# Optimization experiments

Hardware: AMD Instinct MI355X
Metric: run time of the kernel (lower is better)

Reference implementation:

```python
import jax, jax.numpy as jnp
import numpy as np

B, N, D = 4, 4096, 256

def setup_inputs() -> dict:
    key = jax.random.key(0)
    k1, = jax.random.split(key, 1)
    x = jax.random.normal(k1, (B, N, D), dtype=jnp.float32)
    attn_mask = jnp.ones((B, 1, N), dtype=jnp.int32)
    pad_mask = jnp.ones((B, 1, N), dtype=jnp.int32)
    return {"x": x, "attn_mask": attn_mask, "pad_mask": pad_mask, "dim_": D}

def reference(x, attn_mask, pad_mask, dim_):
    # adj is None -> scores = x @ x^T / sqrt(d)
    scale = jnp.sqrt(jnp.asarray(x.shape[-1], x.dtype))
    scores = jnp.einsum('bnd,bmd->bnm', x, x) / scale  # [B, N, N]
    # NOTE: original calls non-in-place masked_fill and discards the result,
    # so pad_mask / attn_mask have no effect on the output (faithful).
    prob = jax.nn.softmax(scores, axis=-1)
    # dropout is identity in inference mode
    return jnp.einsum('bnm,bmd->bnd', prob, x)
```

## Files before the change

kernel.cpp:

```cpp
#include <hip/hip_runtime.h>

typedef __attribute__((ext_vector_type(8))) short short8;
typedef __attribute__((ext_vector_type(4))) float f32x4;
typedef __attribute__((ext_vector_type(4))) unsigned int u32x4;
typedef __attribute__((ext_vector_type(2))) long long2_t;

#define NTOK 4096
#define DIM  256
#define P_STRIDE 72
#define KS_ROW 272
#define KS_TILE 17408
#define KT_TILE 16384
#define KSF8_BYTES (4u * 64u * KS_TILE)

__device__ __forceinline__ unsigned pack2bf(float a, float b) {
  unsigned ua = __builtin_bit_cast(unsigned, a) + 0x8000u;
  unsigned ub = __builtin_bit_cast(unsigned, b) + 0x8000u;
  return __builtin_amdgcn_perm(ub, ua, 0x07060302u);
}

__global__ __launch_bounds__(256, 4)
void prep_kernel(const float* __restrict__ X, unsigned char* __restrict__ Ws) {
  unsigned char*  Ksf8 = Ws;
  unsigned short* KtImg = (unsigned short*)(Ws + KSF8_BYTES);
  const int b    = blockIdx.x & 3;
  const int sub  = blockIdx.x >> 2;
  const int t    = sub >> 3;
  const int part = sub & 7;
  const int tid  = threadIdx.x;
  const float* src = X + ((size_t)b * NTOK + t * 64) * DIM;
  unsigned char* dstK = Ksf8 + (size_t)(b * 64 + t) * KS_TILE;
  #pragma unroll
  for (int i = 0; i < 3; ++i) {
    int idx = tid + i * 256;
    if (idx < 544) {
      int rl = idx / 68, w = idx % 68;
      if (w < 64) {
        int r = part * 8 + rl;
        int ds2 = w >> 4, rem = (w & 15) << 2;
        int quad = rem >> 4, rem2 = rem & 15;
        int half = rem2 >> 3, j0 = rem2 & 7;
        int d0 = (2 * ds2 + half) * 32 + quad * 8 + j0;
        const float* s = src + r * DIM + d0;
        int u = 0;
        u = __builtin_amdgcn_cvt_pk_fp8_f32(s[0], s[1], u, false);
        u = __builtin_amdgcn_cvt_pk_fp8_f32(s[2], s[3], u, true);
        *(int*)(dstK + r * KS_ROW + w * 4) = u;
      }
    }
  }
  {
    const int d = tid;
    float f[8];
    #pragma unroll
    for (int i = 0; i < 8; ++i) f[i] = src[(part * 8 + i) * DIM + d];
    union { unsigned u[4]; u32x4 v; } p;
    p.u[0] = pack2bf(f[0], f[1]);
    p.u[1] = pack2bf(f[2], f[3]);
    p.u[2] = pack2bf(f[4], f[5]);
    p.u[3] = pack2bf(f[6], f[7]);
    *(u32x4*)(KtImg + ((size_t)(b * 64 + t)) * KT_TILE + part * 2048 + d * 8) = p.v;
  }
}

__device__ __forceinline__ void pv_step(const unsigned short* __restrict__ pr,
                                        const unsigned short* __restrict__ kt,
                                        f32x4 (&o)[4][4],
                                        int ks, int dq, int quad, int ln) {
  const int pos = (ks * 4 + quad) ^ ((ln >> 3) << 1);
  short8 ap[4], bv[4];
  #pragma unroll
  for (int s = 0; s < 4; ++s)
    ap[s] = *(const short8*)(&pr[(s * 16 + ln) * P_STRIDE + (pos << 3)]);
  const unsigned short* kb = kt + (ks * 4 + quad) * 2048 + (dq * 64 + ln) * 8;
  #pragma unroll
  for (int dt = 0; dt < 4; ++dt) bv[dt] = *(const short8*)(kb + dt * 128);
  #pragma unroll
  for (int s = 0; s < 4; ++s)
    #pragma unroll
    for (int dt = 0; dt < 4; ++dt)
      o[s][dt] = __builtin_amdgcn_mfma_f32_16x16x32_bf16(ap[s], bv[dt], o[s][dt], 0, 0, 0);
}

__global__ __launch_bounds__(512, 1)
void fa_kernel(const unsigned char* __restrict__ Ws, float* __restrict__ Out) {
  __shared__ __align__(16) unsigned char  ksb[2][KS_TILE];
  __shared__ __align__(16) unsigned short ktb[2][KT_TILE];
  __shared__ __align__(16) unsigned short pb[2][64 * P_STRIDE];
  __shared__ float lbuf[64][4];

  const unsigned char*  Ksf8 = Ws;
  const unsigned short* KtImg = (const unsigned short*)(Ws + KSF8_BYTES);

  const int tid  = threadIdx.x;
  const int b    = blockIdx.x & 3;
  const int qblk = blockIdx.x >> 2;
  const int wave = tid >> 6;
  const int lane = tid & 63;
  const int ln   = lane & 15;
  const int quad = lane >> 4;
  const int qh   = wave & 1;
  const int kq   = wave >> 1;

  const unsigned char*  ksImgB = Ksf8 + (size_t)b * 64 * KS_TILE;
  const unsigned short* ktImgB = KtImg + (size_t)b * 64 * KT_TILE;

  long aQ[2][8];
  #pragma unroll
  for (int s = 0; s < 2; ++s) {
    const unsigned char* qrow =
        ksImgB + (size_t)qblk * KS_TILE + (qh * 32 + s * 16 + ln) * KS_ROW;
    #pragma unroll
    for (int ds2 = 0; ds2 < 4; ++ds2) {
      long2_t v = *(const long2_t*)(qrow + ds2 * 64 + quad * 16);
      aQ[s][2 * ds2]     = v.x;
      aQ[s][2 * ds2 + 1] = v.y;
    }
  }

  f32x4 o[4][4];
  #pragma unroll
  for (int s = 0; s < 4; ++s)
    #pragma unroll
    for (int dt = 0; dt < 4; ++dt) o[s][dt] = (f32x4)(0.0f);
  float lrow[2][4] = {{0.f,0.f,0.f,0.f},{0.f,0.f,0.f,0.f}};

  const float c2 = 0.0901684400f;
  const int pwPos = ((kq * 2 + (ln >> 3)) ^ ((quad >> 1) << 1)) << 3;
  const int pwCol = ln & 7;

  #pragma unroll
  for (int i = 0; i < 3; ++i) {
    int idx = wave + i * 8;
    if (idx < 17)
      __builtin_amdgcn_global_load_lds(
          (const __attribute__((address_space(1))) unsigned*)(ksImgB + idx * 1024 + lane * 16),
          (__attribute__((address_space(3))) unsigned*)(&ksb[0][idx * 1024 + lane * 16]),
          16, 0, 0);
  }

  for (int t = 0; t < 64; ++t) {
    __syncthreads();
    const int buf = t & 1;

    #pragma unroll
    for (int i = 0; i < 7; ++i) {
      int idx = wave + i * 8;
      if (idx < 17) {
        if (t < 63)
          __builtin_amdgcn_global_load_lds(
              (const __attribute__((address_space(1))) unsigned*)
                  (ksImgB + (size_t)(t + 1) * KS_TILE + idx * 1024 + lane * 16),
              (__attribute__((address_space(3))) unsigned*)(&ksb[buf ^ 1][idx * 1024 + lane * 16]),
              16, 0, 0);
      } else if (idx < 49) {
        int k = idx - 17;
        __builtin_amdgcn_global_load_lds(
            (const __attribute__((address_space(1))) unsigned*)
                ((const unsigned char*)(ktImgB + (size_t)t * KT_TILE) + k * 1024 + lane * 16),
            (__attribute__((address_space(3))) unsigned*)(&ktb[buf][k * 512 + lane * 8]),
            16, 0, 0);
      }
    }

    f32x4 sf0 = (f32x4)(0.0f), sf1 = (f32x4)(0.0f);
    {
      const unsigned char* krow = &ksb[buf][(kq * 16 + ln) * KS_ROW];
      #pragma unroll
      for (int ds2 = 0; ds2 < 4; ++ds2) {
        long2_t bk = *(const long2_t*)(krow + ds2 * 64 + quad * 16);
        sf0 = __builtin_amdgcn_mfma_f32_16x16x32_fp8_fp8(aQ[0][2*ds2],   bk.x, sf0, 0, 0, 0);
        sf0 = __builtin_amdgcn_mfma_f32_16x16x32_fp8_fp8(aQ[0][2*ds2+1], bk.y, sf0, 0, 0, 0);
        sf1 = __builtin_amdgcn_mfma_f32_16x16x32_fp8_fp8(aQ[1][2*ds2],   bk.x, sf1, 0, 0, 0);
        sf1 = __builtin_amdgcn_mfma_f32_16x16x32_fp8_fp8(aQ[1][2*ds2+1], bk.y, sf1, 0, 0, 0);
      }
    }
    {
      unsigned short* pw = pb[buf];
      #pragma unroll
      for (int j = 0; j < 4; ++j) {
        float p0 = __builtin_amdgcn_exp2f(sf0[j] * c2);
        float p1 = __builtin_amdgcn_exp2f(sf1[j] * c2);
        lrow[0][j] += p0;
        lrow[1][j] += p1;
        unsigned q0 = __builtin_bit_cast(unsigned, p0);
        unsigned q1 = __builtin_bit_cast(unsigned, p1);
        unsigned n0 = (unsigned)__builtin_amdgcn_mov_dpp((int)q0, 0xB1, 0xF, 0xF, true);
        unsigned n1 = (unsigned)__builtin_amdgcn_mov_dpp((int)q1, 0xB1, 0xF, 0xF, true);
        if ((ln & 1) == 0) {
          const int r0 = qh * 32 + quad * 4 + j;
          unsigned d0 = pack2bf(__builtin_bit_cast(float, q0), __builtin_bit_cast(float, n0));
          unsigned d1 = pack2bf(__builtin_bit_cast(float, q1), __builtin_bit_cast(float, n1));
          *(unsigned*)(&pw[r0 * P_STRIDE + pwPos + pwCol]) = d0;
          *(unsigned*)(&pw[(r0 + 16) * P_STRIDE + pwPos + pwCol]) = d1;
        }
      }
    }

    if (t > 0)
      pv_step(pb[buf ^ 1], ktb[buf ^ 1], o, qh, kq, quad, ln);
  }

  __syncthreads();
  pv_step(pb[1], ktb[1], o, qh, kq, quad, ln);

  #pragma unroll
  for (int off = 1; off < 16; off <<= 1)
    #pragma unroll
    for (int s = 0; s < 2; ++s)
      #pragma unroll
      for (int j = 0; j < 4; ++j)
        lrow[s][j] += __shfl_xor(lrow[s][j], off, 64);
  if (ln == 0) {
    #pragma unroll
    for (int s = 0; s < 2; ++s)
      #pragma unroll
      for (int j = 0; j < 4; ++j)
        lbuf[qh * 32 + s * 16 + quad * 4 + j][kq] = lrow[s][j];
  }
  __syncthreads();

  float* om = (float*)&ktb[0][0];
  if (qh == 1) {
    #pragma unroll
    for (int s = 0; s < 4; ++s)
      #pragma unroll
      for (int dt = 0; dt < 4; ++dt)
        *(f32x4*)(om + kq * 4096 + (s * 4 + dt) * 256 + lane * 4) = o[s][dt];
  }
  __syncthreads();
  if (qh == 0) {
    float* outp = Out + (size_t)(b * NTOK + qblk * 64) * DIM + kq * 64;
    #pragma unroll
    for (int s = 0; s < 4; ++s) {
      #pragma unroll
      for (int dt = 0; dt < 4; ++dt) {
        f32x4 oo = o[s][dt] + *(const f32x4*)(om + kq * 4096 + (s * 4 + dt) * 256 + lane * 4);
        #pragma unroll
        for (int j = 0; j < 4; ++j) {
          const int row = s * 16 + quad * 4 + j;
          f32x4 lv = *(const f32x4*)lbuf[row];
          outp[(size_t)row * DIM + dt * 16 + ln] = oo[j] / (lv[0] + lv[1] + lv[2] + lv[3]);
        }
      }
    }
  }
}

extern "C" void kernel_launch(void* const* d_in, const int* in_sizes, int n_in,
                              void* d_out, int out_size, void* d_ws, size_t ws_size,
                              hipStream_t stream) {
  const float* X = (const float*)d_in[0];
  float* Out = (float*)d_out;
  unsigned char* Ws = (unsigned char*)d_ws;
  (void)in_sizes; (void)n_in; (void)out_size; (void)ws_size;
  hipLaunchKernelGGL(prep_kernel, dim3(2048), dim3(256), 0, stream, X, Ws);
  hipLaunchKernelGGL(fa_kernel, dim3(256), dim3(512), 0, stream, Ws, Out);
}
```

Baseline: 176.6 us.

## Split key range across two blocks with bf16 partials and atomic-flag merge

Splits each query block's 4096 keys into two halves handled by separate blocks, doubling the grid to 512 blocks. This fills more of the CUs, which the previous 256-block grid left partly idle. Each block writes bf16 partial outputs and fp32 row sums to workspace, and the second block to finish, found through an atomic counter, merges and normalizes them. P/Kt buffering drops from double to single buffered, PV is restructured per wave, and the launch bounds rise to 4 blocks per CU. This adds a memset, extra global traffic, bf16 rounding of partials, and more barriers per iteration.

```diff
diff --git a/kernel.cpp b/kernel.cpp
--- a/kernel.cpp
+++ b/kernel.cpp
@@ -11,18 +11,26 @@
 #define KS_ROW 272
 #define KS_TILE 17408
 #define KT_TILE 16384
-#define KSF8_BYTES (4u * 64u * KS_TILE)
+#define KT_OFF   4456448ull
+#define PART_OFF 12845056ull
+#define LSUM_OFF 29622272ull
+#define FLAG_OFF 29753344ull
 
 __device__ __forceinline__ unsigned pack2bf(float a, float b) {
   unsigned ua = __builtin_bit_cast(unsigned, a) + 0x8000u;
   unsigned ub = __builtin_bit_cast(unsigned, b) + 0x8000u;
   return __builtin_amdgcn_perm(ub, ua, 0x07060302u);
 }
+__device__ __forceinline__ unsigned short f2bf(float f) {
+  unsigned u = __builtin_bit_cast(unsigned, f);
+  u += 0x7fffu + ((u >> 16) & 1u);
+  return (unsigned short)(u >> 16);
+}
 
 __global__ __launch_bounds__(256, 4)
 void prep_kernel(const float* __restrict__ X, unsigned char* __restrict__ Ws) {
   unsigned char*  Ksf8 = Ws;
-  unsigned short* KtImg = (unsigned short*)(Ws + KSF8_BYTES);
+  unsigned short* KtImg = (unsigned short*)(Ws + KT_OFF);
   const int b    = blockIdx.x & 3;
   const int sub  = blockIdx.x >> 2;
   const int t    = sub >> 3;
@@ -65,36 +73,41 @@
 
 __device__ __forceinline__ void pv_step(const unsigned short* __restrict__ pr,
                                         const unsigned short* __restrict__ kt,
-                                        f32x4 (&o)[4][4],
-                                        int ks, int dq, int quad, int ln) {
-  const int pos = (ks * 4 + quad) ^ ((ln >> 3) << 1);
-  short8 ap[4], bv[4];
-  #pragma unroll
-  for (int s = 0; s < 4; ++s)
-    ap[s] = *(const short8*)(&pr[(s * 16 + ln) * P_STRIDE + (pos << 3)]);
-  const unsigned short* kb = kt + (ks * 4 + quad) * 2048 + (dq * 64 + ln) * 8;
-  #pragma unroll
-  for (int dt = 0; dt < 4; ++dt) bv[dt] = *(const short8*)(kb + dt * 128);
-  #pragma unroll
-  for (int s = 0; s < 4; ++s)
-    #pragma unroll
-    for (int dt = 0; dt < 4; ++dt)
-      o[s][dt] = __builtin_amdgcn_mfma_f32_16x16x32_bf16(ap[s], bv[dt], o[s][dt], 0, 0, 0);
-}
-
-__global__ __launch_bounds__(512, 1)
-void fa_kernel(const unsigned char* __restrict__ Ws, float* __restrict__ Out) {
+                                        f32x4 (&o)[2][4],
+                                        int qh, int dq, int quad, int ln) {
+  #pragma unroll
+  for (int ks = 0; ks < 2; ++ks) {
+    const int pos = (ks * 4 + quad) ^ ((ln >> 3) << 1);
+    short8 ap[2], bv[4];
+    #pragma unroll
+    for (int s = 0; s < 2; ++s)
+      ap[s] = *(const short8*)(&pr[(qh * 32 + s * 16 + ln) * P_STRIDE + (pos << 3)]);
+    const unsigned short* kb = kt + (ks * 4 + quad) * 2048 + (dq * 64 + ln) * 8;
+    #pragma unroll
+    for (int dt = 0; dt < 4; ++dt) bv[dt] = *(const short8*)(kb + dt * 128);
+    #pragma unroll
+    for (int s = 0; s < 2; ++s)
+      #pragma unroll
+      for (int dt = 0; dt < 4; ++dt)
+        o[s][dt] = __builtin_amdgcn_mfma_f32_16x16x32_bf16(ap[s], bv[dt], o[s][dt], 0, 0, 0);
+  }
+}
+
+__global__ __launch_bounds__(512, 4)
+void fa_kernel(unsigned char* __restrict__ Ws, float* __restrict__ Out) {
   __shared__ __align__(16) unsigned char  ksb[2][KS_TILE];
-  __shared__ __align__(16) unsigned short ktb[2][KT_TILE];
-  __shared__ __align__(16) unsigned short pb[2][64 * P_STRIDE];
+  __shared__ __align__(16) unsigned short ktb[KT_TILE];
+  __shared__ __align__(16) unsigned short pb[64 * P_STRIDE];
   __shared__ float lbuf[64][4];
-
-  const unsigned char*  Ksf8 = Ws;
-  const unsigned short* KtImg = (const unsigned short*)(Ws + KSF8_BYTES);
+  __shared__ int who;
+
+  const unsigned char*  Ksf8  = Ws;
+  const unsigned short* KtImg = (const unsigned short*)(Ws + KT_OFF);
 
   const int tid  = threadIdx.x;
   const int b    = blockIdx.x & 3;
-  const int qblk = blockIdx.x >> 2;
+  const int kh   = (blockIdx.x >> 2) & 1;
+  const int qblk = blockIdx.x >> 3;
   const int wave = tid >> 6;
   const int lane = tid & 63;
   const int ln   = lane & 15;
@@ -102,14 +115,14 @@
   const int qh   = wave & 1;
   const int kq   = wave >> 1;
 
-  const unsigned char*  ksImgB = Ksf8 + (size_t)b * 64 * KS_TILE;
-  const unsigned short* ktImgB = KtImg + (size_t)b * 64 * KT_TILE;
+  const unsigned char*  ksT = Ksf8 + (size_t)(b * 64 + kh * 32) * KS_TILE;
+  const unsigned short* ktT = KtImg + (size_t)(b * 64 + kh * 32) * KT_TILE;
 
   long aQ[2][8];
   #pragma unroll
   for (int s = 0; s < 2; ++s) {
     const unsigned char* qrow =
-        ksImgB + (size_t)qblk * KS_TILE + (qh * 32 + s * 16 + ln) * KS_ROW;
+        Ksf8 + (size_t)(b * 64 + qblk) * KS_TILE + (qh * 32 + s * 16 + ln) * KS_ROW;
     #pragma unroll
     for (int ds2 = 0; ds2 < 4; ++ds2) {
       long2_t v = *(const long2_t*)(qrow + ds2 * 64 + quad * 16);
@@ -118,9 +131,9 @@
     }
   }
 
-  f32x4 o[4][4];
-  #pragma unroll
-  for (int s = 0; s < 4; ++s)
+  f32x4 o[2][4];
+  #pragma unroll
+  for (int s = 0; s < 2; ++s)
     #pragma unroll
     for (int dt = 0; dt < 4; ++dt) o[s][dt] = (f32x4)(0.0f);
   float lrow[2][4] = {{0.f,0.f,0.f,0.f},{0.f,0.f,0.f,0.f}};
@@ -134,12 +147,14 @@
     int idx = wave + i * 8;
     if (idx < 17)
       __builtin_amdgcn_global_load_lds(
-          (const __attribute__((address_space(1))) unsigned*)(ksImgB + idx * 1024 + lane * 16),
+          (const __attribute__((address_space(1))) unsigned*)(ksT + idx * 1024 + lane * 16),
           (__attribute__((address_space(3))) unsigned*)(&ksb[0][idx * 1024 + lane * 16]),
           16, 0, 0);
   }
 
-  for (int t = 0; t < 64; ++t) {
+  for (int t = 0; t < 32; ++t) {
+    __syncthreads();
+    if (t > 0) pv_step(pb, ktb, o, qh, kq, quad, ln);
     __syncthreads();
     const int buf = t & 1;
 
@@ -147,18 +162,18 @@
     for (int i = 0; i < 7; ++i) {
       int idx = wave + i * 8;
       if (idx < 17) {
-        if (t < 63)
+        if (t < 31)
           __builtin_amdgcn_global_load_lds(
               (const __attribute__((address_space(1))) unsigned*)
-                  (ksImgB + (size_t)(t + 1) * KS_TILE + idx * 1024 + lane * 16),
+                  (ksT + (size_t)(t + 1) * KS_TILE + idx * 1024 + lane * 16),
               (__attribute__((address_space(3))) unsigned*)(&ksb[buf ^ 1][idx * 1024 + lane * 16]),
               16, 0, 0);
       } else if (idx < 49) {
         int k = idx - 17;
         __builtin_amdgcn_global_load_lds(
             (const __attribute__((address_space(1))) unsigned*)
-                ((const unsigned char*)(ktImgB + (size_t)t * KT_TILE) + k * 1024 + lane * 16),
-            (__attribute__((address_space(3))) unsigned*)(&ktb[buf][k * 512 + lane * 8]),
+                ((const unsigned char*)ktT + (size_t)t * 32768 + k * 1024 + lane * 16),
+            (__attribute__((address_space(3))) unsigned*)(&ktb[k * 512 + lane * 8]),
             16, 0, 0);
       }
     }
@@ -175,34 +190,28 @@
         sf1 = __builtin_amdgcn_mfma_f32_16x16x32_fp8_fp8(aQ[1][2*ds2+1], bk.y, sf1, 0, 0, 0);
       }
     }
-    {
-      unsigned short* pw = pb[buf];
-      #pragma unroll
-      for (int j = 0; j < 4; ++j) {
-        float p0 = __builtin_amdgcn_exp2f(sf0[j] * c2);
-        float p1 = __builtin_amdgcn_exp2f(sf1[j] * c2);
-        lrow[0][j] += p0;
-        lrow[1][j] += p1;
-        unsigned q0 = __builtin_bit_cast(unsigned, p0);
-        unsigned q1 = __builtin_bit_cast(unsigned, p1);
-        unsigned n0 = (unsigned)__builtin_amdgcn_mov_dpp((int)q0, 0xB1, 0xF, 0xF, true);
-        unsigned n1 = (unsigned)__builtin_amdgcn_mov_dpp((int)q1, 0xB1, 0xF, 0xF, true);
-        if ((ln & 1) == 0) {
-          const int r0 = qh * 32 + quad * 4 + j;
-          unsigned d0 = pack2bf(__builtin_bit_cast(float, q0), __builtin_bit_cast(float, n0));
-          unsigned d1 = pack2bf(__builtin_bit_cast(float, q1), __builtin_bit_cast(float, n1));
-          *(unsigned*)(&pw[r0 * P_STRIDE + pwPos + pwCol]) = d0;
-          *(unsigned*)(&pw[(r0 + 16) * P_STRIDE + pwPos + pwCol]) = d1;
-        }
-      }
-    }
-
-    if (t > 0)
-      pv_step(pb[buf ^ 1], ktb[buf ^ 1], o, qh, kq, quad, ln);
-  }
-
-  __syncthreads();
-  pv_step(pb[1], ktb[1], o, qh, kq, quad, ln);
+    #pragma unroll
+    for (int j = 0; j < 4; ++j) {
+      float p0 = __builtin_amdgcn_exp2f(sf0[j] * c2);
+      float p1 = __builtin_amdgcn_exp2f(sf1[j] * c2);
+      lrow[0][j] += p0;
+      lrow[1][j] += p1;
+      unsigned q0 = __builtin_bit_cast(unsigned, p0);
+      unsigned q1 = __builtin_bit_cast(unsigned, p1);
+      unsigned n0 = (unsigned)__builtin_amdgcn_mov_dpp((int)q0, 0xB1, 0xF, 0xF, true);
+      unsigned n1 = (unsigned)__builtin_amdgcn_mov_dpp((int)q1, 0xB1, 0xF, 0xF, true);
+      if ((ln & 1) == 0) {
+        const int r0 = qh * 32 + quad * 4 + j;
+        unsigned d0 = pack2bf(__builtin_bit_cast(float, q0), __builtin_bit_cast(float, n0));
+        unsigned d1 = pack2bf(__builtin_bit_cast(float, q1), __builtin_bit_cast(float, n1));
+        *(unsigned*)(&pb[r0 * P_STRIDE + pwPos + pwCol]) = d0;
+        *(unsigned*)(&pb[(r0 + 16) * P_STRIDE + pwPos + pwCol]) = d1;
+      }
+    }
+  }
+
+  __syncthreads();
+  pv_step(pb, ktb, o, qh, kq, quad, ln);
 
   #pragma unroll
   for (int off = 1; off < 16; off <<= 1)
@@ -220,29 +229,57 @@
   }
   __syncthreads();
 
-  float* om = (float*)&ktb[0][0];
-  if (qh == 1) {
-    #pragma unroll
-    for (int s = 0; s < 4; ++s)
-      #pragma unroll
-      for (int dt = 0; dt < 4; ++dt)
-        *(f32x4*)(om + kq * 4096 + (s * 4 + dt) * 256 + lane * 4) = o[s][dt];
-  }
-  __syncthreads();
-  if (qh == 0) {
-    float* outp = Out + (size_t)(b * NTOK + qblk * 64) * DIM + kq * 64;
-    #pragma unroll
-    for (int s = 0; s < 4; ++s) {
-      #pragma unroll
-      for (int dt = 0; dt < 4; ++dt) {
-        f32x4 oo = o[s][dt] + *(const f32x4*)(om + kq * 4096 + (s * 4 + dt) * 256 + lane * 4);
-        #pragma unroll
-        for (int j = 0; j < 4; ++j) {
-          const int row = s * 16 + quad * 4 + j;
-          f32x4 lv = *(const f32x4*)lbuf[row];
-          outp[(size_t)row * DIM + dt * 16 + ln] = oo[j] / (lv[0] + lv[1] + lv[2] + lv[3]);
-        }
-      }
+  float* lsumAll = (float*)(Ws + LSUM_OFF);
+  float* lsumMe  = lsumAll + ((size_t)(kh * 4 + b) * 64 + qblk) * 64;
+  if (tid < 64) {
+    f32x4 lv = *(const f32x4*)lbuf[tid];
+    lsumMe[tid] = lv[0] + lv[1] + lv[2] + lv[3];
+  }
+  unsigned short* pAll = (unsigned short*)(Ws + PART_OFF);
+  unsigned short* pMe  = pAll + ((size_t)(kh * 4 + b) * 64 + qblk) * (64 * 256);
+  #pragma unroll
+  for (int s = 0; s < 2; ++s)
+    #pragma unroll
+    for (int dt = 0; dt < 4; ++dt)
+      #pragma unroll
+      for (int j = 0; j < 4; ++j)
+        pMe[(qh * 32 + s * 16 + quad * 4 + j) * 256 + kq * 64 + dt * 16 + ln] = f2bf(o[s][dt][j]);
+
+  __threadfence();
+  __syncthreads();
+  if (tid == 0)
+    who = atomicAdd((int*)(Ws + FLAG_OFF) + (b * 64 + qblk), 1);
+  __syncthreads();
+
+  if (who == 1) {
+    __threadfence();
+    const unsigned short* pA = pAll + ((size_t)(0 * 4 + b) * 64 + qblk) * (64 * 256);
+    const unsigned short* pB = pAll + ((size_t)(1 * 4 + b) * 64 + qblk) * (64 * 256);
+    const float* lA = lsumAll + ((size_t)(0 * 4 + b) * 64 + qblk) * 64;
+    const float* lB = lsumAll + ((size_t)(1 * 4 + b) * 64 + qblk) * 64;
+    float* outp = Out + ((size_t)b * NTOK + qblk * 64) * DIM;
+    #pragma unroll
+    for (int c = 0; c < 4; ++c) {
+      int idx8 = c * 512 + tid;
+      int e = idx8 * 8;
+      int row = e >> 8;
+      u32x4 va = *(const u32x4*)(pA + e);
+      u32x4 vb = *(const u32x4*)(pB + e);
+      float rl = 1.0f / (lA[row] + lB[row]);
+      f32x4 o0, o1;
+      #pragma unroll
+      for (int k = 0; k < 4; ++k) {
+        float a_lo = __builtin_bit_cast(float, va[k] << 16);
+        float a_hi = __builtin_bit_cast(float, va[k] & 0xffff0000u);
+        float b_lo = __builtin_bit_cast(float, vb[k] << 16);
+        float b_hi = __builtin_bit_cast(float, vb[k] & 0xffff0000u);
+        float vlo = (a_lo + b_lo) * rl;
+        float vhi = (a_hi + b_hi) * rl;
+        if (k < 2) { o0[2*k] = vlo; o0[2*k+1] = vhi; }
+        else       { o1[2*(k-2)] = vlo; o1[2*(k-2)+1] = vhi; }
+      }
+      *(f32x4*)(outp + e)     = o0;
+      *(f32x4*)(outp + e + 4) = o1;
     }
   }
 }
@@ -254,6 +291,7 @@
   float* Out = (float*)d_out;
   unsigned char* Ws = (unsigned char*)d_ws;
   (void)in_sizes; (void)n_in; (void)out_size; (void)ws_size;
+  hipMemsetAsync(Ws + FLAG_OFF, 0, 1024, stream);
   hipLaunchKernelGGL(prep_kernel, dim3(2048), dim3(256), 0, stream, X, Ws);
-  hipLaunchKernelGGL(fa_kernel, dim3(256), dim3(512), 0, stream, Ws, Out);
-}
+  hipLaunchKernelGGL(fa_kernel, dim3(512), dim3(512), 0, stream, Ws, Out);
+}
```

After: 381.4 us. 116% more time.
